# Kernel optimization log

Hardware: AMD Instinct MI355X
Metric: run time of the kernel (lower is better)

## Reference

```python
import jax, jax.numpy as jnp
import numpy as np

NDIM = 2
NSIG = 2
NCELLS = 1000
BATCH = 4
DT = 1e-3
NSTEPS = 251  # 1 + int((t1 - t0)/dt) with t0=0, t1=0.25
SIGMA = 1e-3


def _phi(y, pw1, pb1, pw2, pb2, pw3, pb3, pw4, pb4, pw5, pb5):
    # phi_nn: 2 -> 16 -> 32 -> 32 -> 16 -> 1 with tanh activations
    h = jnp.tanh(y @ pw1.T + pb1)
    h = jnp.tanh(h @ pw2.T + pb2)
    h = jnp.tanh(h @ pw3.T + pb3)
    h = jnp.tanh(h @ pw4.T + pb4)
    return h @ pw5.T + pb5  # (ncells, 1)


def setup_inputs() -> dict:
    key = jax.random.key(0)
    ks = jax.random.split(key, 16)
    # x = [t0, t1, y0.flat, tcrit, p0(2), p1(2)] per batch item
    y0 = 0.1 * jax.random.normal(ks[0], (BATCH, NCELLS, NDIM), dtype=jnp.float32)
    t0 = jnp.zeros((BATCH, 1), jnp.float32)
    t1 = jnp.full((BATCH, 1), 0.25, jnp.float32)
    tcrit = jnp.full((BATCH, 1), 0.125, jnp.float32)
    p0 = jax.random.normal(ks[1], (BATCH, 2), dtype=jnp.float32)
    p1 = jax.random.normal(ks[2], (BATCH, 2), dtype=jnp.float32)
    x = jnp.concatenate([t0, t1, y0.reshape(BATCH, -1), tcrit, p0, p1], axis=1)
    # Wiener increments ~ N(0, dt)
    dw = np.sqrt(DT).astype(np.float32) * jax.random.normal(
        ks[3], (BATCH, NSTEPS, NCELLS, NDIM), dtype=jnp.float32)
    # phi_nn weights (torch Linear: weight is (out, in)), init N(0, 0.1), bias 0
    def w(k, o, i):
        return 0.1 * jax.random.normal(k, (o, i), dtype=jnp.float32)
    inp = dict(x=x, dw=dw,
               pw1=w(ks[4], 16, 2), pb1=jnp.zeros(16, jnp.float32),
               pw2=w(ks[5], 32, 16), pb2=jnp.zeros(32, jnp.float32),
               pw3=w(ks[6], 32, 32), pb3=jnp.zeros(32, jnp.float32),
               pw4=w(ks[7], 16, 32), pb4=jnp.zeros(16, jnp.float32),
               pw5=w(ks[8], 1, 16), pb5=jnp.zeros(1, jnp.float32),
               tw=w(ks[9], NDIM, NSIG), tb=jnp.zeros(NDIM, jnp.float32))
    return inp


def reference(x, dw, pw1, pb1, pw2, pb2, pw3, pb3, pw4, pb4, pw5, pb5, tw, tb):
    phi_params = (pw1, pb1, pw2, pb2, pw3, pb3, pw4, pb4, pw5, pb5)
    grad_phi = jax.grad(lambda yy: jnp.sum(_phi(yy, *phi_params)))

    def simulate(xi, dwi):
        t0 = xi[0]
        y0 = xi[2:2 + NCELLS * NDIM].reshape(NCELLS, NDIM)
        ps = xi[2 + NCELLS * NDIM:]
        tcrit, p0, p1 = ps[0], ps[1:3], ps[3:5]
        ts = t0 + DT * jnp.arange(NSTEPS, dtype=xi.dtype)

        def step(y, t_dw):
            t, dwt = t_dw
            sig = jnp.where(t < tcrit, p0, p1)      # step signal f_signal(t, params)
            tilt = sig @ tw.T + tb                  # grad_tilt: (ndim,)
            drift = -(grad_phi(y) + tilt)           # f(t, y)
            y_new = y + drift * DT + SIGMA * dwt    # Euler-Maruyama
            return y_new, None

        y_final, _ = jax.lax.scan(step, y0, (ts, dwi))
        return y_final

    return jax.vmap(simulate)(x, dw)  # (BATCH, NCELLS, NDIM)
```

## Files before the change

### kernel.cpp

```cpp
#include <hip/hip_runtime.h>

#define NDIMC 2
#define NCELLS 1000
#define BATCHSZ 4
#define NSTEPS 251
#define XROW 2007

typedef float v2f __attribute__((ext_vector_type(2)));
typedef float v4f __attribute__((ext_vector_type(4)));

__device__ __forceinline__ v2f vlo(v4f v) { return __builtin_shufflevector(v, v, 0, 1); }
__device__ __forceinline__ v2f vhi(v4f v) { return __builtin_shufflevector(v, v, 2, 3); }

__device__ __forceinline__ v2f pfma(v2f w, v2f v, v2f a) {
    return __builtin_elementwise_fma(w, v, a);
}

__device__ __forceinline__ float fast_tanh(float x) {
    float e = __builtin_amdgcn_exp2f(x * 2.885390081777926774f);
    float r = __builtin_amdgcn_rcpf(e + 1.0f);
    return fmaf(-2.0f, r, 1.0f);
}


template<int CTRL>
__device__ __forceinline__ float dpp_mov(float x) {
    return __int_as_float(__builtin_amdgcn_update_dpp(
        0, __float_as_int(x), CTRL, 0xf, 0xf, true));
}
template<int CTRL>
__device__ __forceinline__ float dpp_add(float z) { return z + dpp_mov<CTRL>(z); }

__device__ __forceinline__ float row16_sum(float z) {
    z = dpp_add<0xB1>(z);
    z = dpp_add<0x1B>(z);
    z = dpp_add<0x141>(z);
    z = dpp_add<0x140>(z);
    return z;
}

struct G16 { v2f p[8]; };
__device__ __forceinline__ G16 gather16(float z) {
    G16 g;
    const float v0 = z;
    const float v1 = dpp_mov<0x4E>(v0);
    const float v2 = dpp_mov<0x141>(v0);
    const float v3 = dpp_mov<0x141>(v1);
    const float v4 = dpp_mov<0x140>(v0);
    const float v5 = dpp_mov<0x140>(v1);
    const float v6 = dpp_mov<0x140>(v2);
    const float v7 = dpp_mov<0x140>(v3);
    g.p[0] = v2f{v0, dpp_mov<0xB1>(v0)};
    g.p[1] = v2f{v1, dpp_mov<0xB1>(v1)};
    g.p[2] = v2f{v2, dpp_mov<0xB1>(v2)};
    g.p[3] = v2f{v3, dpp_mov<0xB1>(v3)};
    g.p[4] = v2f{v4, dpp_mov<0xB1>(v4)};
    g.p[5] = v2f{v5, dpp_mov<0xB1>(v5)};
    g.p[6] = v2f{v6, dpp_mov<0xB1>(v6)};
    g.p[7] = v2f{v7, dpp_mov<0xB1>(v7)};
    return g;
}

__device__ __forceinline__ float gdot16(const v2f (&w)[8], const G16& g, float bias) {
    v2f a0 = {bias, 0.f}, a1 = {0.f, 0.f}, a2 = {0.f, 0.f}, a3 = {0.f, 0.f};
    a0 = pfma(w[0], g.p[0], a0); a1 = pfma(w[1], g.p[1], a1);
    a2 = pfma(w[2], g.p[2], a2); a3 = pfma(w[3], g.p[3], a3);
    a0 = pfma(w[4], g.p[4], a0); a1 = pfma(w[5], g.p[5], a1);
    a2 = pfma(w[6], g.p[6], a2); a3 = pfma(w[7], g.p[7], a3);
    v2f s = (a0 + a1) + (a2 + a3);
    return s[0] + s[1];
}

__device__ __forceinline__ float pdot32(const v2f (&w)[16], const float* p, float bias) {
    v2f a0 = {bias, 0.f}, a1 = {0.f, 0.f}, a2 = {0.f, 0.f}, a3 = {0.f, 0.f};
    #pragma unroll
    for (int c = 0; c < 2; ++c) {
        v4f u0 = *(const v4f*)(p + c * 16);
        v4f u1 = *(const v4f*)(p + c * 16 + 4);
        v4f u2 = *(const v4f*)(p + c * 16 + 8);
        v4f u3 = *(const v4f*)(p + c * 16 + 12);
        a0 = pfma(w[c*8+0], vlo(u0), a0); a1 = pfma(w[c*8+1], vhi(u0), a1);
        a2 = pfma(w[c*8+2], vlo(u1), a2); a3 = pfma(w[c*8+3], vhi(u1), a3);
        a0 = pfma(w[c*8+4], vlo(u2), a0); a1 = pfma(w[c*8+5], vhi(u2), a1);
        a2 = pfma(w[c*8+6], vlo(u3), a2); a3 = pfma(w[c*8+7], vhi(u3), a3);
    }
    v2f s = (a0 + a1) + (a2 + a3);
    return s[0] + s[1];
}

__global__ __launch_bounds__(64, 2)
void phinn_sde_kernel(const float* __restrict__ x,   const float* __restrict__ dw,
                      const float* __restrict__ pw1, const float* __restrict__ pb1,
                      const float* __restrict__ pw2, const float* __restrict__ pb2,
                      const float* __restrict__ pw3, const float* __restrict__ pb3,
                      const float* __restrict__ pw4, const float* __restrict__ pb4,
                      const float* __restrict__ pw5, const float* __restrict__ pb5,
                      const float* __restrict__ tw,  const float* __restrict__ tb,
                      float* __restrict__ out)
{
    __shared__ __align__(16) float sh[2][4][32];

    const int tid  = threadIdx.x;
    const int n    = tid & 31;
    const int grp  = tid >> 5;
    const int s16  = n & 15;
    const int b    = blockIdx.x / (NCELLS / 2);
    const int pair = blockIdx.x % (NCELLS / 2);
    const int cell = pair * 2 + grp;

    const int TAU[8] = {0, 2, 7, 5, 15, 13, 8, 10};

    const float r1a = pw1[s16 * 2 + 0];
    const float r1b = pw1[s16 * 2 + 1];
    const float rb1 = pb1[s16];
    const float rb2 = pb2[n];
    const float rb3 = pb3[n];
    const float rb4 = pb4[s16];
    const float rw5 = pw5[s16];

    v2f w2f[8], w4b[8];
    #pragma unroll
    for (int t = 0; t < 8; ++t) {
        const int j0 = s16 ^ TAU[t];
        const int j1 = j0 ^ 1;
        w2f[t] = v2f{pw2[n * 16 + j0], pw2[n * 16 + j1]};
        w4b[t] = v2f{pw4[j0 * 32 + n], pw4[j1 * 32 + n]};
    }

    v2f w3p[16];
    #pragma unroll
    for (int j = 0; j < 16; ++j) w3p[j] = ((const v2f*)pw3)[n * 16 + j];

    v2f w4p[16];
    #pragma unroll
    for (int j = 0; j < 16; ++j) w4p[j] = ((const v2f*)pw4)[s16 * 16 + j];

    v2f w3cp[16];
    #pragma unroll
    for (int j = 0; j < 16; ++j)
        w3cp[j] = v2f{pw3[(2*j) * 32 + n], pw3[(2*j+1) * 32 + n]};

    v2f w2cp[16];
    #pragma unroll
    for (int j = 0; j < 16; ++j)
        w2cp[j] = v2f{pw2[(2*j) * 16 + s16], pw2[(2*j+1) * 16 + s16]};

    const float* xb = x + (size_t)b * XROW;
    const float t0v    = xb[0];
    const float tcritv = xb[2 + NCELLS * NDIMC];
    const float p0x = xb[2003], p0y = xb[2004];
    const float p1x = xb[2005], p1y = xb[2006];
    const float tA0 = fmaf(p0x, tw[0], fmaf(p0y, tw[1], tb[0]));
    const float tA1 = fmaf(p0x, tw[2], fmaf(p0y, tw[3], tb[1]));
    const float tB0 = fmaf(p1x, tw[0], fmaf(p1y, tw[1], tb[0]));
    const float tB1 = fmaf(p1x, tw[2], fmaf(p1y, tw[3], tb[1]));

    float y0 = xb[2 + cell * 2 + 0];
    float y1 = xb[2 + cell * 2 + 1];

    const float* dwb = dw + (size_t)b * NSTEPS * NCELLS * NDIMC
                          + (size_t)pair * 2 * NDIMC;
    int dwoff = grp * NDIMC;

    const float* l0 = &sh[grp][0][0];
    const float* l1 = &sh[grp][1][0];
    const float* l2 = &sh[grp][2][0];
    const float* l3 = &sh[grp][3][0];

    #pragma unroll 1
    for (int i = 0; i < NSTEPS; ++i) {
        const float2 dwv = *(const float2*)(dwb + dwoff);
        dwoff += NCELLS * NDIMC;
        const float t = t0v + 0.001f * (float)i;

        const float h1 = fast_tanh(fmaf(r1a, y0, fmaf(r1b, y1, rb1)));

        const G16 G1 = gather16(h1);
        const float h2 = fast_tanh(gdot16(w2f, G1, rb2));
        sh[grp][0][n] = h2;

        const float h3 = fast_tanh(pdot32(w3p, l0, rb3));
        sh[grp][1][n] = h3;

        const float h4 = fast_tanh(pdot32(w4p, l1, rb4));

        const float g4p = rw5 * fmaf(-h4, h4, 1.0f);

        const G16 G4 = gather16(g4p);
        const float g3p = gdot16(w4b, G4, 0.f) * fmaf(-h3, h3, 1.0f);
        sh[grp][2][n] = g3p;

        const float g2p = pdot32(w3cp, l2, 0.f) * fmaf(-h2, h2, 1.0f);
        sh[grp][3][n] = g2p;

        const float g1p = pdot32(w2cp, l3, 0.f) * fmaf(-h1, h1, 1.0f);

        const float v0 = row16_sum(r1a * g1p);
        const float v1 = row16_sum(r1b * g1p);

        const bool  cnd   = t < tcritv;
        const float tilt0 = cnd ? tA0 : tB0;
        const float tilt1 = cnd ? tA1 : tB1;
        y0 = fmaf(-0.001f, v0 + tilt0, fmaf(0.001f, dwv.x, y0));
        y1 = fmaf(-0.001f, v1 + tilt1, fmaf(0.001f, dwv.y, y1));
    }

    if (n == 0) {
        *(float2*)(out + ((size_t)b * NCELLS + cell) * NDIMC) = make_float2(y0, y1);
    }
}

extern "C" void kernel_launch(void* const* d_in, const int* in_sizes, int n_in,
                              void* d_out, int out_size, void* d_ws, size_t ws_size,
                              hipStream_t stream) {
    const float* x   = (const float*)d_in[0];
    const float* dw  = (const float*)d_in[1];
    const float* pw1 = (const float*)d_in[2];
    const float* pb1 = (const float*)d_in[3];
    const float* pw2 = (const float*)d_in[4];
    const float* pb2 = (const float*)d_in[5];
    const float* pw3 = (const float*)d_in[6];
    const float* pb3 = (const float*)d_in[7];
    const float* pw4 = (const float*)d_in[8];
    const float* pb4 = (const float*)d_in[9];
    const float* pw5 = (const float*)d_in[10];
    const float* pb5 = (const float*)d_in[11];
    const float* tw  = (const float*)d_in[12];
    const float* tb  = (const float*)d_in[13];
    float* out = (float*)d_out;

    dim3 grid(BATCHSZ * NCELLS / 2);
    dim3 block(64);
    phinn_sde_kernel<<<grid, block, 0, stream>>>(x, dw, pw1, pb1, pw2, pb2,
                                                 pw3, pb3, pw4, pb4, pw5, pb5,
                                                 tw, tb, out);
}
```

Baseline: 283.7 us.

## Replace LDS round trips in layers 4 and backward-1 with DPP/permlane16 reductions

Layer 4's forward pass and the layer-2 backward step are restructured. Instead of staging activations through shared memory, each half-row computes a 16-wide partial dot product using DPP gathers and combines the two halves with v_permlane16_swap. The pw5 scaling is folded into the precomputed transposed pw4 weights, which also cuts the backward layer-4 product to an 8-wide half dot. This removes two LDS store/load round trips per step and their implied waits, and shrinks weight register arrays. The cost is extra cross-lane permute instructions, and it depends on the gfx950 permlane16_swap instruction.

```diff
diff --git a/kernel.cpp b/kernel.cpp
--- a/kernel.cpp
+++ b/kernel.cpp
@@ -37,6 +37,12 @@
     z = dpp_add<0x141>(z);
     z = dpp_add<0x140>(z);
     return z;
+}
+
+__device__ __forceinline__ float xor16(float z, bool odd) {
+    float t = z, u = z;
+    asm("v_permlane16_swap_b32 %0, %1" : "+v"(t), "+v"(u));
+    return odd ? t : u;
 }
 
 struct G16 { v2f p[8]; };
@@ -71,6 +77,16 @@
     return s[0] + s[1];
 }
 
+__device__ __forceinline__ float pdot8h(const v2f (&w)[4], const float* p) {
+    v4f u0 = *(const v4f*)(p);
+    v4f u1 = *(const v4f*)(p + 4);
+    v2f a0 = {0.f, 0.f}, a1 = {0.f, 0.f};
+    a0 = pfma(w[0], vlo(u0), a0); a1 = pfma(w[1], vhi(u0), a1);
+    a0 = pfma(w[2], vlo(u1), a0); a1 = pfma(w[3], vhi(u1), a1);
+    v2f s = a0 + a1;
+    return s[0] + s[1];
+}
+
 __device__ __forceinline__ float pdot32(const v2f (&w)[16], const float* p, float bias) {
     v2f a0 = {bias, 0.f}, a1 = {0.f, 0.f}, a2 = {0.f, 0.f}, a3 = {0.f, 0.f};
     #pragma unroll
@@ -98,12 +114,14 @@
                       const float* __restrict__ tw,  const float* __restrict__ tb,
                       float* __restrict__ out)
 {
-    __shared__ __align__(16) float sh[2][4][32];
+    __shared__ __align__(16) float sh[2][3][32];
 
     const int tid  = threadIdx.x;
     const int n    = tid & 31;
     const int grp  = tid >> 5;
     const int s16  = n & 15;
+    const int hi   = n >> 4;
+    const bool odd = hi;
     const int b    = blockIdx.x / (NCELLS / 2);
     const int pair = blockIdx.x % (NCELLS / 2);
     const int cell = pair * 2 + grp;
@@ -116,34 +134,33 @@
     const float rb2 = pb2[n];
     const float rb3 = pb3[n];
     const float rb4 = pb4[s16];
-    const float rw5 = pw5[s16];
-
-    v2f w2f[8], w4b[8];
+
+    v2f w2f[8], w4f[8], w2cp[8];
     #pragma unroll
     for (int t = 0; t < 8; ++t) {
         const int j0 = s16 ^ TAU[t];
         const int j1 = j0 ^ 1;
-        w2f[t] = v2f{pw2[n * 16 + j0], pw2[n * 16 + j1]};
-        w4b[t] = v2f{pw4[j0 * 32 + n], pw4[j1 * 32 + n]};
+        const int k0 = hi * 16 + j0;
+        const int k1 = hi * 16 + j1;
+        w2f[t]  = v2f{pw2[n * 16 + j0],   pw2[n * 16 + j1]};
+        w4f[t]  = v2f{pw4[s16 * 32 + k0], pw4[s16 * 32 + k1]};
+        w2cp[t] = v2f{pw2[k0 * 16 + s16], pw2[k1 * 16 + s16]};
     }
 
     v2f w3p[16];
     #pragma unroll
     for (int j = 0; j < 16; ++j) w3p[j] = ((const v2f*)pw3)[n * 16 + j];
 
-    v2f w4p[16];
-    #pragma unroll
-    for (int j = 0; j < 16; ++j) w4p[j] = ((const v2f*)pw4)[s16 * 16 + j];
+    v2f w4cp[4];
+    #pragma unroll
+    for (int j = 0; j < 4; ++j)
+        w4cp[j] = v2f{pw4[(hi*8 + 2*j)     * 32 + n] * pw5[hi*8 + 2*j],
+                      pw4[(hi*8 + 2*j + 1) * 32 + n] * pw5[hi*8 + 2*j + 1]};
 
     v2f w3cp[16];
     #pragma unroll
     for (int j = 0; j < 16; ++j)
         w3cp[j] = v2f{pw3[(2*j) * 32 + n], pw3[(2*j+1) * 32 + n]};
-
-    v2f w2cp[16];
-    #pragma unroll
-    for (int j = 0; j < 16; ++j)
-        w2cp[j] = v2f{pw2[(2*j) * 16 + s16], pw2[(2*j+1) * 16 + s16]};
 
     const float* xb = x + (size_t)b * XROW;
     const float t0v    = xb[0];
@@ -165,7 +182,6 @@
     const float* l0 = &sh[grp][0][0];
     const float* l1 = &sh[grp][1][0];
     const float* l2 = &sh[grp][2][0];
-    const float* l3 = &sh[grp][3][0];
 
     #pragma unroll 1
     for (int i = 0; i < NSTEPS; ++i) {
@@ -180,20 +196,23 @@
         sh[grp][0][n] = h2;
 
         const float h3 = fast_tanh(pdot32(w3p, l0, rb3));
-        sh[grp][1][n] = h3;
-
-        const float h4 = fast_tanh(pdot32(w4p, l1, rb4));
-
-        const float g4p = rw5 * fmaf(-h4, h4, 1.0f);
-
-        const G16 G4 = gather16(g4p);
-        const float g3p = gdot16(w4b, G4, 0.f) * fmaf(-h3, h3, 1.0f);
+
+        const G16 G3 = gather16(h3);
+        const float A4 = gdot16(w4f, G3, 0.f);
+        const float h4 = fast_tanh(A4 + xor16(A4, odd) + rb4);
+
+        const float d4 = fmaf(-h4, h4, 1.0f);
+        sh[grp][1][n] = d4;
+
+        const float q3 = pdot8h(w4cp, l1 + hi * 8);
+        const float g3p = (q3 + xor16(q3, odd)) * fmaf(-h3, h3, 1.0f);
         sh[grp][2][n] = g3p;
 
         const float g2p = pdot32(w3cp, l2, 0.f) * fmaf(-h2, h2, 1.0f);
-        sh[grp][3][n] = g2p;
-
-        const float g1p = pdot32(w2cp, l3, 0.f) * fmaf(-h1, h1, 1.0f);
+
+        const G16 G6 = gather16(g2p);
+        const float A1 = gdot16(w2cp, G6, 0.f);
+        const float g1p = (A1 + xor16(A1, odd)) * fmaf(-h1, h1, 1.0f);
 
         const float v0 = row16_sum(r1a * g1p);
         const float v1 = row16_sum(r1b * g1p);
```

Measured after the change: 252.3 us (median of 2 runs). -11.1%, faster.
